# Kernel optimization log

Measured on AMD Instinct MI355X. Metric: run time of the kernel, lower is better.

The kernel has to match this reference:

```python
import math
import jax, jax.numpy as jnp
import numpy as np

D = 512; H = 8; N = 6; DFF = 2048; VS = 32000; VT = 32000
B = 4; S = 1024; T = 1024
EPS = 1e-5


def _pe(length, d):
    pos = jnp.arange(length, dtype=jnp.float32)[:, None]
    div = jnp.exp(jnp.arange(0, d, 2, dtype=jnp.float32) * (-math.log(10000.0) / d))
    pe = jnp.zeros((length, d), jnp.float32)
    pe = pe.at[:, 0::2].set(jnp.sin(pos * div)).at[:, 1::2].set(jnp.cos(pos * div))
    return pe  # [L, D]


def _ln(x, g, b):
    m = x.mean(-1, keepdims=True)
    v = ((x - m) ** 2).mean(-1, keepdims=True)
    return (x - m) / jnp.sqrt(v + EPS) * g + b


def _mha(xq, xkv, w, b, mask):
    # w: [4, D, D], b: [4, D]; mask broadcastable to [B, H, Sq, Sk]
    nb, sq, d = xq.shape
    dk = d // H
    def proj(x, i):
        return (x @ w[i] + b[i]).reshape(x.shape[0], x.shape[1], H, dk).transpose(0, 2, 1, 3)
    q, k, v = proj(xq, 0), proj(xkv, 1), proj(xkv, 2)
    scores = jnp.einsum('bhqd,bhkd->bhqk', q, k) / math.sqrt(dk)
    scores = jnp.where(mask == 0, -1e9, scores)
    p = jax.nn.softmax(scores, axis=-1)
    o = jnp.einsum('bhqk,bhkd->bhqd', p, v).transpose(0, 2, 1, 3).reshape(nb, sq, d)
    return o @ w[3] + b[3]


def _ffn(x, w1, b1, w2, b2):
    return jax.nn.relu(x @ w1 + b1) @ w2 + b2


def _forward(src_emb, tgt_emb,
             enc_attn_w, enc_attn_b, enc_ffn_w1, enc_ffn_b1, enc_ffn_w2, enc_ffn_b2,
             enc_ln_g, enc_ln_b, enc_fg, enc_fb,
             dec_self_w, dec_self_b, dec_src_w, dec_src_b,
             dec_ffn_w1, dec_ffn_b1, dec_ffn_w2, dec_ffn_b2,
             dec_ln_g, dec_ln_b, dec_fg, dec_fb,
             gen_w, gen_b,
             src, tgt, src_mask, tgt_mask):
    # embed + positional encoding (dropout off: eval mode)
    x = src_emb[src] + _pe(src.shape[1], D)[None]
    for i in range(N):
        a = _mha(x, x, enc_attn_w[i], enc_attn_b[i], src_mask)
        x = _ln(x + a, enc_ln_g[i, 0], enc_ln_b[i, 0])
        f = _ffn(x, enc_ffn_w1[i], enc_ffn_b1[i], enc_ffn_w2[i], enc_ffn_b2[i])
        x = _ln(x + f, enc_ln_g[i, 1], enc_ln_b[i, 1])
    memory = _ln(x, enc_fg, enc_fb)

    y = tgt_emb[tgt] + _pe(tgt.shape[1], D)[None]
    for i in range(N):
        a = _mha(y, y, dec_self_w[i], dec_self_b[i], tgt_mask)
        y = _ln(y + a, dec_ln_g[i, 0], dec_ln_b[i, 0])
        a = _mha(y, memory, dec_src_w[i], dec_src_b[i], src_mask)
        y = _ln(y + a, dec_ln_g[i, 1], dec_ln_b[i, 1])
        f = _ffn(y, dec_ffn_w1[i], dec_ffn_b1[i], dec_ffn_w2[i], dec_ffn_b2[i])
        y = _ln(y + f, dec_ln_g[i, 2], dec_ln_b[i, 2])
    y = _ln(y, dec_fg, dec_fb)
    return y @ gen_w + gen_b  # [B, T, VT]


def setup_inputs():
    key = jax.random.key(0)
    ks = iter(jax.random.split(key, 48))
    def w(*shape):
        return jax.random.normal(next(ks), shape, dtype=jnp.float32) * 0.02
    inp = {}
    inp['src_emb'] = w(VS, D)
    inp['tgt_emb'] = w(VT, D)
    inp['enc_attn_w'] = w(N, 4, D, D)
    inp['enc_attn_b'] = jnp.zeros((N, 4, D), jnp.float32)
    inp['enc_ffn_w1'] = w(N, D, DFF)
    inp['enc_ffn_b1'] = jnp.zeros((N, DFF), jnp.float32)
    inp['enc_ffn_w2'] = w(N, DFF, D)
    inp['enc_ffn_b2'] = jnp.zeros((N, D), jnp.float32)
    inp['enc_ln_g'] = jnp.ones((N, 2, D), jnp.float32)
    inp['enc_ln_b'] = jnp.zeros((N, 2, D), jnp.float32)
    inp['enc_fg'] = jnp.ones((D,), jnp.float32)
    inp['enc_fb'] = jnp.zeros((D,), jnp.float32)
    inp['dec_self_w'] = w(N, 4, D, D)
    inp['dec_self_b'] = jnp.zeros((N, 4, D), jnp.float32)
    inp['dec_src_w'] = w(N, 4, D, D)
    inp['dec_src_b'] = jnp.zeros((N, 4, D), jnp.float32)
    inp['dec_ffn_w1'] = w(N, D, DFF)
    inp['dec_ffn_b1'] = jnp.zeros((N, DFF), jnp.float32)
    inp['dec_ffn_w2'] = w(N, DFF, D)
    inp['dec_ffn_b2'] = jnp.zeros((N, D), jnp.float32)
    inp['dec_ln_g'] = jnp.ones((N, 3, D), jnp.float32)
    inp['dec_ln_b'] = jnp.zeros((N, 3, D), jnp.float32)
    inp['dec_fg'] = jnp.ones((D,), jnp.float32)
    inp['dec_fb'] = jnp.zeros((D,), jnp.float32)
    inp['gen_w'] = w(D, VT)
    inp['gen_b'] = jnp.zeros((VT,), jnp.float32)
    inp['src'] = jax.random.randint(next(ks), (B, S), 0, VS)
    inp['tgt'] = jax.random.randint(next(ks), (B, T), 0, VT)
    inp['src_mask'] = jnp.ones((B, 1, 1, S), jnp.int32)
    inp['tgt_mask'] = jnp.tril(jnp.ones((T, T), jnp.int32))[None, None]  # causal [1,1,T,T]
    return inp


def reference(src_emb, tgt_emb, enc_attn_w, enc_attn_b, enc_ffn_w1, enc_ffn_b1,
              enc_ffn_w2, enc_ffn_b2, enc_ln_g, enc_ln_b, enc_fg, enc_fb,
              dec_self_w, dec_self_b, dec_src_w, dec_src_b,
              dec_ffn_w1, dec_ffn_b1, dec_ffn_w2, dec_ffn_b2,
              dec_ln_g, dec_ln_b, dec_fg, dec_fb, gen_w, gen_b,
              src, tgt, src_mask, tgt_mask):
    return _forward(src_emb, tgt_emb, enc_attn_w, enc_attn_b, enc_ffn_w1, enc_ffn_b1,
                    enc_ffn_w2, enc_ffn_b2, enc_ln_g, enc_ln_b, enc_fg, enc_fb,
                    dec_self_w, dec_self_b, dec_src_w, dec_src_b,
                    dec_ffn_w1, dec_ffn_b1, dec_ffn_w2, dec_ffn_b2,
                    dec_ln_g, dec_ln_b, dec_fg, dec_fb, gen_w, gen_b,
                    src, tgt, src_mask, tgt_mask)
```

## Files before the change

### kernel.cpp

```cpp
#include <hip/hip_runtime.h>


typedef __bf16 bf16x8 __attribute__((ext_vector_type(8)));
typedef __bf16 bf16x4 __attribute__((ext_vector_type(4)));
typedef float  f32x4  __attribute__((ext_vector_type(4)));

__device__ __forceinline__ void gload_lds16(const void* g, void* l) {
  __builtin_amdgcn_global_load_lds((__attribute__((address_space(1))) void*)g,
                                   (__attribute__((address_space(3))) void*)l,
                                   16, 0, 0);
}

__device__ __forceinline__ void hard_barrier() {
  asm volatile("" ::: "memory");
  __builtin_amdgcn_sched_barrier(0);
  __builtin_amdgcn_s_barrier();
  __builtin_amdgcn_sched_barrier(0);
  asm volatile("" ::: "memory");
}

__global__ __launch_bounds__(512, 2)
void gemm256_kernel(const __bf16* __restrict__ A, int lda,
                    const __bf16* __restrict__ BT, int ldb,
                    float* __restrict__ C, int ldc,
                    const float* __restrict__ bias, int K)
{
  __shared__ char ldsraw[131072];
  const int tid  = threadIdx.x;
  const int lane = tid & 63, wid = tid >> 6;
  const int wr = wid >> 2, wc = wid & 3;
  const int bm = blockIdx.x * 256, bn = blockIdx.y * 256;

  auto stage = [&](int slot, int kt) {
    const char* Ag = (const char*)A;
    const char* Bg = (const char*)BT;
    char* base = ldsraw + slot * 65536;
    const long long k0b = (long long)kt * 128;
#pragma unroll
    for (int i = 0; i < 4; i++) {
      int t = tid + i * 512;
      int row = t >> 3, cb = (t & 7) << 4;
      int src = cb ^ ((row & 7) << 4);
      gload_lds16(Ag + ((long long)(bm + row) * lda) * 2 + k0b + src, base + t * 16);
    }
#pragma unroll
    for (int i = 0; i < 4; i++) {
      int t = tid + i * 512;
      int row = t >> 3, cb = (t & 7) << 4;
      int src = cb ^ ((row & 7) << 4);
      gload_lds16(Bg + ((long long)(bn + row) * ldb) * 2 + k0b + src,
                  base + 32768 + t * 16);
    }
  };

  f32x4 acc[8][4] = {};
  const int NT = K / 64;

  stage(0, 0);
  stage(1, 1);

  for (int kt = 0; kt < NT; kt++) {
    if (kt < NT - 1) {
      asm volatile("s_waitcnt vmcnt(8)" ::: "memory");
    } else {
      asm volatile("s_waitcnt vmcnt(0)" ::: "memory");
    }
    hard_barrier();
    const char* sA = ldsraw + (kt & 1) * 65536;
    const char* sB = sA + 32768;
#pragma unroll
    for (int q = 0; q < 4; q++) {
      const int qr = q >> 1, qc = q & 1;
      bf16x8 af[4][2], bf[2][2];
#pragma unroll
      for (int i = 0; i < 4; i++) {
        int row = wr * 128 + (qr * 4 + i) * 16 + (lane & 15);
#pragma unroll
        for (int kk = 0; kk < 2; kk++) {
          int g = kk * 64 + (lane >> 4) * 16;
          af[i][kk] = *(const bf16x8*)(sA + row * 128 + (g ^ ((row & 7) << 4)));
        }
      }
#pragma unroll
      for (int j = 0; j < 2; j++) {
        int row = wc * 64 + (qc * 2 + j) * 16 + (lane & 15);
#pragma unroll
        for (int kk = 0; kk < 2; kk++) {
          int g = kk * 64 + (lane >> 4) * 16;
          bf[j][kk] = *(const bf16x8*)(sB + row * 128 + (g ^ ((row & 7) << 4)));
        }
      }
      __builtin_amdgcn_s_barrier();
      asm volatile("s_waitcnt lgkmcnt(0)" ::: "memory");
      __builtin_amdgcn_sched_barrier(0);
      __builtin_amdgcn_s_setprio(1);
#pragma unroll
      for (int kk = 0; kk < 2; kk++)
#pragma unroll
        for (int i = 0; i < 4; i++)
#pragma unroll
          for (int j = 0; j < 2; j++)
            acc[qr * 4 + i][qc * 2 + j] = __builtin_amdgcn_mfma_f32_16x16x32_bf16(
                af[i][kk], bf[j][kk], acc[qr * 4 + i][qc * 2 + j], 0, 0, 0);
      __builtin_amdgcn_s_setprio(0);
    }
    hard_barrier();
    if (kt + 2 < NT) stage(kt & 1, kt + 2);
  }

  float* ct = (float*)ldsraw;
#pragma unroll
  for (int c = 0; c < 4; c++) {
    __syncthreads();
    if (wr == (c >> 1)) {
      const int ib = (c & 1) * 4;
#pragma unroll
      for (int i = 0; i < 4; i++) {
#pragma unroll
        for (int j = 0; j < 4; j++) {
          int lrow = i * 16 + (lane >> 4) * 4;
          int lcol = wc * 64 + j * 16 + (lane & 15);
          float bv = bias[bn + lcol];
#pragma unroll
          for (int r = 0; r < 4; r++)
            ct[(lrow + r) * 260 + lcol] = acc[ib + i][j][r] + bv;
        }
      }
    }
    __syncthreads();
#pragma unroll
    for (int it = 0; it < 8; it++) {
      int idx = tid + it * 512;
      int row = idx >> 6, c4 = (idx & 63) * 4;
      f32x4 v = *(const f32x4*)(ct + row * 260 + c4);
      *(f32x4*)(C + (long long)(bm + c * 64 + row) * ldc + bn + c4) = v;
    }
  }
}

template<int EPI>
__global__ __launch_bounds__(256)
void gemm2_kernel(const __bf16* __restrict__ A, const __bf16* __restrict__ Akv,
                  int lda,
                  const __bf16* __restrict__ BT, int ldb,
                  void* __restrict__ Cv, int ldc,
                  const float* __restrict__ bias, int K,
                  __bf16* __restrict__ qb, __bf16* __restrict__ kb,
                  __bf16* __restrict__ vt)
{
  constexpr int BM = 128, BN = 128, BK = 64;
  constexpr int WM = 64, WN = 64, FM = 4, FN = 4;
  constexpr int SLOT = 2 * BM * BK;
  __shared__ char ldsraw[65536];
  __bf16* lds = (__bf16*)ldsraw;
  const int tid  = threadIdx.x;
  const int lane = tid & 63, wave = tid >> 6;
  const int wr = wave >> 1, wc = wave & 1;
  const int bm = blockIdx.x * BM, bn = blockIdx.y * BN;
  const __bf16* Ause = (EPI == 2 && blockIdx.y >= 4) ? Akv : A;

  auto stage = [&](int slot, int kt) {
    const char* Ag = (const char*)Ause;
    const char* Bg = (const char*)BT;
    char* base = (char*)(lds + slot * SLOT);
    const long long k0b = (long long)kt * (BK * 2);
#pragma unroll
    for (int i = 0; i < 4; i++) {
      int t = tid + i * 256;
      int row = t >> 3, cb = (t & 7) << 4;
      int src = cb ^ ((row & 7) << 4);
      gload_lds16(Ag + ((long long)(bm + row) * lda) * 2 + k0b + src, base + t * 16);
    }
#pragma unroll
    for (int i = 0; i < 4; i++) {
      int t = tid + i * 256;
      int row = t >> 3, cb = (t & 7) << 4;
      int src = cb ^ ((row & 7) << 4);
      gload_lds16(Bg + ((long long)(bn + row) * ldb) * 2 + k0b + src,
                  base + BM * BK * 2 + t * 16);
    }
  };

  f32x4 acc[FM][FN] = {};
  const int NT = K / BK;

  stage(0, 0);
  stage(1, 1);

  for (int t = 0; t < NT; t++) {
    if (t < NT - 1) {
      asm volatile("s_waitcnt vmcnt(8)" ::: "memory");
    } else {
      asm volatile("s_waitcnt vmcnt(0)" ::: "memory");
    }
    hard_barrier();
    const char* sA = (const char*)(lds + (t & 1) * SLOT);
    const char* sB = sA + BM * BK * 2;
#pragma unroll
    for (int kk = 0; kk < 2; kk++) {
      const int g = kk * 64 + (lane >> 4) * 16;
      bf16x8 af[FM], bfr[FN];
#pragma unroll
      for (int i = 0; i < FM; i++) {
        int row = wr * WM + i * 16 + (lane & 15);
        af[i] = *(const bf16x8*)(sA + row * 128 + (g ^ ((row & 7) << 4)));
      }
#pragma unroll
      for (int j = 0; j < FN; j++) {
        int row = wc * WN + j * 16 + (lane & 15);
        bfr[j] = *(const bf16x8*)(sB + row * 128 + (g ^ ((row & 7) << 4)));
      }
      __builtin_amdgcn_s_setprio(1);
#pragma unroll
      for (int i = 0; i < FM; i++)
#pragma unroll
        for (int j = 0; j < FN; j++)
          acc[i][j] = __builtin_amdgcn_mfma_f32_16x16x32_bf16(af[i], bfr[j], acc[i][j], 0, 0, 0);
      __builtin_amdgcn_s_setprio(0);
    }
    hard_barrier();
    if (t + 2 < NT) stage(t & 1, t + 2);
  }

#pragma unroll
  for (int i = 0; i < FM; i++) {
#pragma unroll
    for (int j = 0; j < FN; j++) {
      int row0 = bm + wr * WM + i * 16 + (lane >> 4) * 4;
      int col  = bn + wc * WN + j * 16 + (lane & 15);
      float bv = bias ? bias[col] : 0.f;
      if constexpr (EPI == 2) {
        int z = col >> 9;
        int cw = col & 511;
        int b = row0 >> 10, s = row0 & 1023;
        int h = cw >> 6, dk = cw & 63;
        long long bh = b * 8 + h;
        if (z == 2) {
          bf16x4 vv;
#pragma unroll
          for (int r = 0; r < 4; r++) vv[r] = (__bf16)(acc[i][j][r] + bv);
          *(bf16x4*)(vt + (bh << 16) + (dk << 10) + s) = vv;
        } else {
          __bf16* dst = (z == 0) ? qb : kb;
          float sc = (z == 0) ? 0.125f : 1.0f;
#pragma unroll
          for (int r = 0; r < 4; r++)
            dst[(bh << 16) + ((long long)(s + r) << 6) + dk] = (__bf16)((acc[i][j][r] + bv) * sc);
        }
      } else {
        __bf16* C = (__bf16*)Cv;
#pragma unroll
        for (int r = 0; r < 4; r++)
          C[(long long)(row0 + r) * ldc + col] = (__bf16)fmaxf(acc[i][j][r] + bv, 0.f);
      }
    }
  }
}

__global__ __launch_bounds__(256)
void gemm_kernel(const __bf16* __restrict__ A, int lda,
                 const __bf16* __restrict__ BT, int ldb,
                 const __bf16* __restrict__ Xbase,
                 __bf16* __restrict__ Xs, int ldc,
                 const float* __restrict__ bias, int K)
{
  constexpr int BM = 128, BN = 64, BK = 64;
  constexpr int WM = 64, WN = 32, FM = 4, FN = 2;
  constexpr int LA = (BM * BK) / 2048;
  constexpr int LB = (BN * BK) / 2048;
  constexpr int SLOT = (BM + BN) * BK;
  __shared__ __bf16 lds[3 * SLOT];
  const int tid  = threadIdx.x;
  const int lane = tid & 63, wave = tid >> 6;
  const int wr = wave >> 1, wc = wave & 1;
  const int bm = blockIdx.x * BM, bn = blockIdx.y * BN;

  auto stage = [&](int slot, int kt) {
    const char* Ag = (const char*)A;
    const char* Bg = (const char*)BT;
    char* base = (char*)(lds + slot * SLOT);
    const long long k0b = (long long)kt * (BK * 2);
#pragma unroll
    for (int i = 0; i < LA; i++) {
      int t = tid + i * 256;
      int row = t >> 3, cb = (t & 7) << 4;
      int src = cb ^ ((row & 7) << 4);
      gload_lds16(Ag + ((long long)(bm + row) * lda) * 2 + k0b + src, base + t * 16);
    }
#pragma unroll
    for (int i = 0; i < LB; i++) {
      int t = tid + i * 256;
      int row = t >> 3, cb = (t & 7) << 4;
      int src = cb ^ ((row & 7) << 4);
      gload_lds16(Bg + ((long long)(bn + row) * ldb) * 2 + k0b + src,
                  base + BM * BK * 2 + t * 16);
    }
  };

  f32x4 acc[FM][FN] = {};
  const int NT = K / BK;

  stage(0, 0);
  stage(1, 1);

  for (int t = 0; t < NT; t++) {
    if (t < NT - 1) {
      asm volatile("s_waitcnt vmcnt(6)" ::: "memory");
    } else {
      asm volatile("s_waitcnt vmcnt(0)" ::: "memory");
    }
    hard_barrier();
    if (t + 2 < NT) stage((t + 2) % 3, t + 2);
    const char* sA = (const char*)(lds + (t % 3) * SLOT);
    const char* sB = sA + BM * BK * 2;
#pragma unroll
    for (int kk = 0; kk < 2; kk++) {
      const int g = kk * 64 + (lane >> 4) * 16;
      bf16x8 af[FM], bfr[FN];
#pragma unroll
      for (int i = 0; i < FM; i++) {
        int row = wr * WM + i * 16 + (lane & 15);
        af[i] = *(const bf16x8*)(sA + row * 128 + (g ^ ((row & 7) << 4)));
      }
#pragma unroll
      for (int j = 0; j < FN; j++) {
        int row = wc * WN + j * 16 + (lane & 15);
        bfr[j] = *(const bf16x8*)(sB + row * 128 + (g ^ ((row & 7) << 4)));
      }
      __builtin_amdgcn_s_setprio(1);
#pragma unroll
      for (int i = 0; i < FM; i++)
#pragma unroll
        for (int j = 0; j < FN; j++)
          acc[i][j] = __builtin_amdgcn_mfma_f32_16x16x32_bf16(af[i], bfr[j], acc[i][j], 0, 0, 0);
      __builtin_amdgcn_s_setprio(0);
    }
  }

#pragma unroll
  for (int i = 0; i < FM; i++) {
#pragma unroll
    for (int j = 0; j < FN; j++) {
      int row0 = bm + wr * WM + i * 16 + (lane >> 4) * 4;
      int col  = bn + wc * WN + j * 16 + (lane & 15);
      float bv = bias[col];
#pragma unroll
      for (int r = 0; r < 4; r++) {
        long long off = (long long)(row0 + r) * ldc + col;
        Xs[off] = (__bf16)(acc[i][j][r] + bv + (float)Xbase[off]);
      }
    }
  }
}

template<int CAUSAL>
__global__ __launch_bounds__(256)
void flash_kernel(const __bf16* __restrict__ qb, const __bf16* __restrict__ kb,
                  const __bf16* __restrict__ vt, const int* __restrict__ smask,
                  __bf16* __restrict__ Ob)
{
  __shared__ __bf16 lK[2 * 128 * 64];
  __shared__ __bf16 lV[2 * 64 * 128];
  __shared__ __bf16 lP[4][16 * 128];
  const int bh = blockIdx.y;
  const int b = bh >> 3, h = bh & 7;
  const int qt = CAUSAL ? ((blockIdx.y < 16) ? blockIdx.x : 15 - blockIdx.x)
                        : blockIdx.x;
  const int q0 = qt * 64;
  const int tid = threadIdx.x, lane = tid & 63, w = tid >> 6;
  const char* kh = (const char*)(kb + ((long long)bh << 16));
  const char* vh = (const char*)(vt + ((long long)bh << 16));

  auto stageKV = [&](int buf, int t) {
    int k0 = t * 128;
#pragma unroll
    for (int i = 0; i < 4; i++) {
      int c = tid + i * 256;
      int row = c >> 3, cb = (c & 7) << 4;
      int cl = cb ^ ((row & 7) << 4);
      gload_lds16(kh + (long long)(k0 + row) * 128 + cl, (char*)lK + buf * 16384 + c * 16);
    }
#pragma unroll
    for (int i = 0; i < 4; i++) {
      int c = tid + i * 256;
      int row = c >> 4, cb = (c & 15) << 4;
      int cl = cb ^ ((row & 7) << 4);
      gload_lds16(vh + (long long)row * 2048 + (long long)k0 * 2 + cl, (char*)lV + buf * 16384 + c * 16);
    }
  };

  bf16x8 qa[2];
  {
    const __bf16* qrow = qb + ((long long)bh << 16)
                       + (long long)(q0 + w * 16 + (lane & 15)) * 64 + (lane >> 4) * 8;
    qa[0] = *(const bf16x8*)(qrow);
    qa[1] = *(const bf16x8*)(qrow + 32);
  }
  f32x4 oacc[4] = {};
  float m[4], l[4];
#pragma unroll
  for (int r = 0; r < 4; r++) { m[r] = -3e38f; l[r] = 0.f; }

  const int nt = CAUSAL ? (qt / 2 + 1) : 8;
  char* lPw = (char*)lP + w * 4096;

  stageKV(0, 0);
  if (nt > 1) stageKV(1, 1);

  for (int t = 0; t < nt; t++) {
    const int k0 = t * 128;
    if (t < nt - 1) {
      asm volatile("s_waitcnt vmcnt(8)" ::: "memory");
    } else {
      asm volatile("s_waitcnt vmcnt(0)" ::: "memory");
    }
    hard_barrier();
    char* cK = (char*)lK + (t & 1) * 16384;
    char* cV = (char*)lV + (t & 1) * 16384;

    f32x4 sf[8];
#pragma unroll
    for (int f = 0; f < 8; f++) {
      int row = f * 16 + (lane & 15);
      f32x4 s = {};
#pragma unroll
      for (int ks = 0; ks < 2; ks++) {
        int cb = ks * 64 + (lane >> 4) * 16;
        bf16x8 kf = *(const bf16x8*)(cK + row * 128 + (cb ^ ((row & 7) << 4)));
        s = __builtin_amdgcn_mfma_f32_16x16x32_bf16(qa[ks], kf, s, 0, 0, 0);
      }
      sf[f] = s;
    }

    if (!CAUSAL) {
#pragma unroll
      for (int f = 0; f < 8; f++) {
        if (smask[b * 1024 + k0 + f * 16 + (lane & 15)] == 0) {
#pragma unroll
          for (int r = 0; r < 4; r++) sf[f][r] = -1e30f;
        }
      }
    } else if (t == nt - 1) {
#pragma unroll
      for (int f = 0; f < 8; f++) {
        int kc = k0 + f * 16 + (lane & 15);
#pragma unroll
        for (int r = 0; r < 4; r++) {
          int qr = q0 + w * 16 + (lane >> 4) * 4 + r;
          if (kc > qr) sf[f][r] = -1e30f;
        }
      }
    }

    float mt[4];
#pragma unroll
    for (int r = 0; r < 4; r++) {
      float v = sf[0][r];
#pragma unroll
      for (int f = 1; f < 8; f++) v = fmaxf(v, sf[f][r]);
      mt[r] = v;
    }
#pragma unroll
    for (int o = 1; o < 16; o <<= 1)
#pragma unroll
      for (int r = 0; r < 4; r++) mt[r] = fmaxf(mt[r], __shfl_xor(mt[r], o));

    bool need = false;
#pragma unroll
    for (int r = 0; r < 4; r++) need = need || (mt[r] > m[r] + 8.f);
    if (__any(need)) {
      float mn[4], cr[4];
#pragma unroll
      for (int r = 0; r < 4; r++) {
        mn[r] = fmaxf(m[r], mt[r]);
        cr[r] = __expf(m[r] - mn[r]);
        m[r]  = mn[r];
        l[r] *= cr[r];
      }
#pragma unroll
      for (int d = 0; d < 4; d++)
#pragma unroll
        for (int r = 0; r < 4; r++) oacc[d][r] *= cr[r];
    }
    float rs[4] = {0.f, 0.f, 0.f, 0.f};
#pragma unroll
    for (int f = 0; f < 8; f++)
#pragma unroll
      for (int r = 0; r < 4; r++) {
        float p = __expf(sf[f][r] - m[r]);
        sf[f][r] = p;
        rs[r] += p;
      }
#pragma unroll
    for (int o = 1; o < 16; o <<= 1)
#pragma unroll
      for (int r = 0; r < 4; r++) rs[r] += __shfl_xor(rs[r], o);
#pragma unroll
    for (int r = 0; r < 4; r++) l[r] += rs[r];

#pragma unroll
    for (int f = 0; f < 8; f++) {
      int colB = f * 32 + (lane & 15) * 2;
#pragma unroll
      for (int r = 0; r < 4; r++) {
        int row = (lane >> 4) * 4 + r;
        *(__bf16*)(lPw + row * 256 + (colB ^ ((row & 7) << 4))) = (__bf16)sf[f][r];
      }
    }
    asm volatile("s_waitcnt lgkmcnt(0)" ::: "memory");

#pragma unroll
    for (int ks = 0; ks < 4; ks++) {
      int prow = lane & 15;
      int cb = ks * 64 + (lane >> 4) * 16;
      bf16x8 pa = *(const bf16x8*)(lPw + prow * 256 + (cb ^ ((prow & 7) << 4)));
#pragma unroll
      for (int d = 0; d < 4; d++) {
        int vrow = d * 16 + (lane & 15);
        bf16x8 vf = *(const bf16x8*)(cV + vrow * 256 + (cb ^ ((vrow & 7) << 4)));
        oacc[d] = __builtin_amdgcn_mfma_f32_16x16x32_bf16(pa, vf, oacc[d], 0, 0, 0);
      }
    }
    hard_barrier();
    if (t + 2 < nt) stageKV(t & 1, t + 2);
  }

  float inv[4];
#pragma unroll
  for (int r = 0; r < 4; r++) inv[r] = 1.f / l[r];
#pragma unroll
  for (int d = 0; d < 4; d++)
#pragma unroll
    for (int r = 0; r < 4; r++) {
      long long row = b * 1024 + q0 + w * 16 + (lane >> 4) * 4 + r;
      Ob[row * 512 + h * 64 + d * 16 + (lane & 15)] = (__bf16)(oacc[d][r] * inv[r]);
    }
}

__global__ void transpose_w_kernel(const float* __restrict__ W, __bf16* __restrict__ WT,
                                   int K, int N)
{
  __shared__ float t[32][33];
  long long mz = (long long)blockIdx.z * K * N;
  W += mz; WT += mz;
  int n0 = blockIdx.x * 32, k0 = blockIdx.y * 32;
  int tx = threadIdx.x, ty = threadIdx.y;
#pragma unroll
  for (int i = 0; i < 32; i += 8)
    t[ty + i][tx] = W[(long long)(k0 + ty + i) * N + (n0 + tx)];
  __syncthreads();
#pragma unroll
  for (int i = 0; i < 32; i += 8)
    WT[(long long)(n0 + ty + i) * K + (k0 + tx)] = (__bf16)t[tx][ty + i];
}

__global__ void embed_kernel(const float* __restrict__ emb, const int* __restrict__ idx,
                             __bf16* __restrict__ Xb)
{
  int row = blockIdx.x;
  int s   = row & 1023;
  int tok = idx[row];
  int d0  = threadIdx.x * 4;
  float4 e = *(const float4*)(emb + (long long)tok * 512 + d0);
  const float* ep = (const float*)&e;
  bf16x4 ob;
#pragma unroll
  for (int j = 0; j < 4; j++) {
    int d = d0 + j;
    float div = expf((float)(d & ~1) * (-9.210340371976184f / 512.f));
    float ang = (float)s * div;
    float pe  = (d & 1) ? cosf(ang) : sinf(ang);
    ob[j] = (__bf16)(ep[j] + pe);
  }
  *(bf16x4*)(Xb + (long long)row * 512 + d0) = ob;
}

__global__ __launch_bounds__(256)
void ln_kernel(const __bf16* __restrict__ Xin,
               const float* __restrict__ g, const float* __restrict__ b,
               __bf16* __restrict__ Xbout)
{
  int row = blockIdx.x * 4 + (threadIdx.x >> 6);
  int lane = threadIdx.x & 63;
  long long base = (long long)row * 512 + lane * 8;
  bf16x8 xv = *(const bf16x8*)(Xin + base);
  float x[8];
#pragma unroll
  for (int i = 0; i < 8; i++) x[i] = (float)xv[i];
  float s = 0.f;
#pragma unroll
  for (int i = 0; i < 8; i++) s += x[i];
#pragma unroll
  for (int o = 32; o > 0; o >>= 1) s += __shfl_xor(s, o);
  float mean = s * (1.f / 512.f);
  float v = 0.f;
#pragma unroll
  for (int i = 0; i < 8; i++) { x[i] -= mean; v += x[i] * x[i]; }
#pragma unroll
  for (int o = 32; o > 0; o >>= 1) v += __shfl_xor(v, o);
  float inv = rsqrtf(v * (1.f / 512.f) + 1e-5f);
  int d0 = lane * 8;
  float gg[8], bb[8];
  *(float4*)gg       = *(const float4*)(g + d0);
  *(float4*)(gg + 4) = *(const float4*)(g + d0 + 4);
  *(float4*)bb       = *(const float4*)(b + d0);
  *(float4*)(bb + 4) = *(const float4*)(b + d0 + 4);
  bf16x8 yb;
#pragma unroll
  for (int i = 0; i < 8; i++)
    yb[i] = (__bf16)(x[i] * inv * gg[i] + bb[i]);
  *(bf16x8*)(Xbout + base) = yb;
}

extern "C" void kernel_launch(void* const* d_in, const int* in_sizes, int n_in,
                              void* d_out, int out_size, void* d_ws, size_t ws_size,
                              hipStream_t stream)
{
  (void)in_sizes; (void)n_in; (void)out_size; (void)ws_size;
  const float* src_emb    = (const float*)d_in[0];
  const float* tgt_emb    = (const float*)d_in[1];
  const float* enc_attn_w = (const float*)d_in[2];
  const float* enc_attn_b = (const float*)d_in[3];
  const float* enc_ffn_w1 = (const float*)d_in[4];
  const float* enc_ffn_b1 = (const float*)d_in[5];
  const float* enc_ffn_w2 = (const float*)d_in[6];
  const float* enc_ffn_b2 = (const float*)d_in[7];
  const float* enc_ln_g   = (const float*)d_in[8];
  const float* enc_ln_b   = (const float*)d_in[9];
  const float* enc_fg     = (const float*)d_in[10];
  const float* enc_fb     = (const float*)d_in[11];
  const float* dec_self_w = (const float*)d_in[12];
  const float* dec_self_b = (const float*)d_in[13];
  const float* dec_src_w  = (const float*)d_in[14];
  const float* dec_src_b  = (const float*)d_in[15];
  const float* dec_ffn_w1 = (const float*)d_in[16];
  const float* dec_ffn_b1 = (const float*)d_in[17];
  const float* dec_ffn_w2 = (const float*)d_in[18];
  const float* dec_ffn_b2 = (const float*)d_in[19];
  const float* dec_ln_g   = (const float*)d_in[20];
  const float* dec_ln_b   = (const float*)d_in[21];
  const float* dec_fg     = (const float*)d_in[22];
  const float* dec_fb     = (const float*)d_in[23];
  const float* gen_w      = (const float*)d_in[24];
  const float* gen_b      = (const float*)d_in[25];
  const int*   src        = (const int*)d_in[26];
  const int*   tgt        = (const int*)d_in[27];
  const int*   src_mask   = (const int*)d_in[28];

  float* out = (float*)d_out;

  char* wp = (char*)d_ws;
  auto alloc = [&](size_t bytes) { void* p = (void*)wp; wp += (bytes + 255) & ~(size_t)255; return p; };
  __bf16* TWea = (__bf16*)alloc(24ull * 262144 * 2);
  __bf16* TWe1 = (__bf16*)alloc(6ull * 1048576 * 2);
  __bf16* TWe2 = (__bf16*)alloc(6ull * 1048576 * 2);
  __bf16* TWds = (__bf16*)alloc(24ull * 262144 * 2);
  __bf16* TWdx = (__bf16*)alloc(24ull * 262144 * 2);
  __bf16* TWd1 = (__bf16*)alloc(6ull * 1048576 * 2);
  __bf16* TWd2 = (__bf16*)alloc(6ull * 1048576 * 2);
  __bf16* Xb   = (__bf16*)alloc(4096ull * 512 * 2);
  __bf16* MEMb = (__bf16*)alloc(4096ull * 512 * 2);
  __bf16* Xs   = (__bf16*)alloc(4096ull * 512 * 2);
  __bf16* qb   = (__bf16*)alloc(32ull * 1024 * 64 * 2);
  __bf16* kb   = (__bf16*)alloc(32ull * 1024 * 64 * 2);
  __bf16* vt   = (__bf16*)alloc(32ull * 1024 * 64 * 2);
  __bf16* Ob   = (__bf16*)alloc(4096ull * 512 * 2);
  __bf16* Fb   = qb;
  __bf16* GENT = TWea;

  transpose_w_kernel<<<dim3(16, 16, 24), dim3(32, 8), 0, stream>>>(enc_attn_w, TWea, 512, 512);
  transpose_w_kernel<<<dim3(64, 16, 6),  dim3(32, 8), 0, stream>>>(enc_ffn_w1, TWe1, 512, 2048);
  transpose_w_kernel<<<dim3(16, 64, 6),  dim3(32, 8), 0, stream>>>(enc_ffn_w2, TWe2, 2048, 512);
  transpose_w_kernel<<<dim3(16, 16, 24), dim3(32, 8), 0, stream>>>(dec_self_w, TWds, 512, 512);
  transpose_w_kernel<<<dim3(16, 16, 24), dim3(32, 8), 0, stream>>>(dec_src_w,  TWdx, 512, 512);
  transpose_w_kernel<<<dim3(64, 16, 6),  dim3(32, 8), 0, stream>>>(dec_ffn_w1, TWd1, 512, 2048);
  transpose_w_kernel<<<dim3(16, 64, 6),  dim3(32, 8), 0, stream>>>(dec_ffn_w2, TWd2, 2048, 512);

  auto attention = [&](const __bf16* wt, const float* bptr, int causal,
                       const __bf16* Aq, const __bf16* Akv) {
    gemm2_kernel<2><<<dim3(32, 12), 256, 0, stream>>>(
        Aq, Akv, 512, wt, 512, nullptr, 0, bptr, 512, qb, kb, vt);
    if (causal)
      flash_kernel<1><<<dim3(16, 32), 256, 0, stream>>>(qb, kb, vt, nullptr, Ob);
    else
      flash_kernel<0><<<dim3(16, 32), 256, 0, stream>>>(qb, kb, vt, src_mask, Ob);
    gemm_kernel<<<dim3(32, 8), 256, 0, stream>>>(
        Ob, 512, wt + 3 * 262144, 512, Xb, Xs, 512, bptr + 3 * 512, 512);
  };

  auto ffn = [&](const __bf16* w1t, const float* b1, const __bf16* w2t, const float* b2) {
    gemm2_kernel<1><<<dim3(32, 16), 256, 0, stream>>>(
        Xb, Xb, 512, w1t, 512, Fb, 2048, b1, 512, nullptr, nullptr, nullptr);
    gemm_kernel<<<dim3(32, 8), 256, 0, stream>>>(
        Fb, 2048, w2t, 2048, Xb, Xs, 512, b2, 2048);
  };

  embed_kernel<<<4096, 128, 0, stream>>>(src_emb, src, Xb);
  for (int i = 0; i < 6; i++) {
    attention(TWea + (long long)i * 1048576, enc_attn_b + i * 2048, 0, Xb, Xb);
    ln_kernel<<<1024, 256, 0, stream>>>(Xs, enc_ln_g + i * 1024, enc_ln_b + i * 1024, Xb);
    ffn(TWe1 + (long long)i * 1048576, enc_ffn_b1 + i * 2048,
        TWe2 + (long long)i * 1048576, enc_ffn_b2 + i * 512);
    ln_kernel<<<1024, 256, 0, stream>>>(Xs, enc_ln_g + i * 1024 + 512, enc_ln_b + i * 1024 + 512, Xb);
  }
  ln_kernel<<<1024, 256, 0, stream>>>(Xb, enc_fg, enc_fb, MEMb);

  transpose_w_kernel<<<dim3(1000, 16, 1), dim3(32, 8), 0, stream>>>(gen_w, GENT, 512, 32000);

  embed_kernel<<<4096, 128, 0, stream>>>(tgt_emb, tgt, Xb);
  for (int i = 0; i < 6; i++) {
    attention(TWds + (long long)i * 1048576, dec_self_b + i * 2048, 1, Xb, Xb);
    ln_kernel<<<1024, 256, 0, stream>>>(Xs, dec_ln_g + i * 1536, dec_ln_b + i * 1536, Xb);

    attention(TWdx + (long long)i * 1048576, dec_src_b + i * 2048, 0, Xb, MEMb);
    ln_kernel<<<1024, 256, 0, stream>>>(Xs, dec_ln_g + i * 1536 + 512, dec_ln_b + i * 1536 + 512, Xb);

    ffn(TWd1 + (long long)i * 1048576, dec_ffn_b1 + i * 2048,
        TWd2 + (long long)i * 1048576, dec_ffn_b2 + i * 512);
    ln_kernel<<<1024, 256, 0, stream>>>(Xs, dec_ln_g + i * 1536 + 1024, dec_ln_b + i * 1536 + 1024, Xb);
  }
  ln_kernel<<<1024, 256, 0, stream>>>(Xb, dec_fg, dec_fb, Xb);

  gemm256_kernel<<<dim3(16, 125), 512, 0, stream>>>(
      Xb, 512, GENT, 512, out, 32000, gen_b, 512);
}
```

Measured before the change: 1.783 ms.

## Replace pipelined GEMMs with smaller-tile single-buffered kernels

Swaps the 256x256 double-buffered generator GEMM for a 128x128 single-buffered kernel, and replaces the 128x64 triple-buffered residual GEMM with a 64x64 single-buffered kernel launched on twice as many blocks. The intent is more blocks and higher occupancy for the small N=512 projections and the vocabulary projection. The trade-off is losing software pipelining (load/compute overlap), barrier-based priority scheduling, and data reuse per tile, so each K step now stalls on global loads.

```diff
diff --git a/kernel.cpp b/kernel.cpp
--- a/kernel.cpp
+++ b/kernel.cpp
@@ -19,101 +19,75 @@
   asm volatile("" ::: "memory");
 }
 
-__global__ __launch_bounds__(512, 2)
-void gemm256_kernel(const __bf16* __restrict__ A, int lda,
-                    const __bf16* __restrict__ BT, int ldb,
-                    float* __restrict__ C, int ldc,
-                    const float* __restrict__ bias, int K)
-{
-  __shared__ char ldsraw[131072];
+__global__ __launch_bounds__(256)
+void gemm_gen_kernel(const __bf16* __restrict__ A, int lda,
+                     const __bf16* __restrict__ BT, int ldb,
+                     float* __restrict__ C, int ldc,
+                     const float* __restrict__ bias, int K)
+{
+  __shared__ char ldsraw[34816];
   const int tid  = threadIdx.x;
-  const int lane = tid & 63, wid = tid >> 6;
-  const int wr = wid >> 2, wc = wid & 3;
-  const int bm = blockIdx.x * 256, bn = blockIdx.y * 256;
-
-  auto stage = [&](int slot, int kt) {
+  const int lane = tid & 63, wave = tid >> 6;
+  const int wr = wave >> 1, wc = wave & 1;
+  const int bm = blockIdx.x * 128, bn = blockIdx.y * 128;
+
+  auto stage = [&](int kt) {
     const char* Ag = (const char*)A;
     const char* Bg = (const char*)BT;
-    char* base = ldsraw + slot * 65536;
     const long long k0b = (long long)kt * 128;
 #pragma unroll
     for (int i = 0; i < 4; i++) {
-      int t = tid + i * 512;
+      int t = tid + i * 256;
       int row = t >> 3, cb = (t & 7) << 4;
       int src = cb ^ ((row & 7) << 4);
-      gload_lds16(Ag + ((long long)(bm + row) * lda) * 2 + k0b + src, base + t * 16);
+      gload_lds16(Ag + ((long long)(bm + row) * lda) * 2 + k0b + src, ldsraw + t * 16);
     }
 #pragma unroll
     for (int i = 0; i < 4; i++) {
-      int t = tid + i * 512;
+      int t = tid + i * 256;
       int row = t >> 3, cb = (t & 7) << 4;
       int src = cb ^ ((row & 7) << 4);
       gload_lds16(Bg + ((long long)(bn + row) * ldb) * 2 + k0b + src,
-                  base + 32768 + t * 16);
+                  ldsraw + 16384 + t * 16);
     }
   };
 
-  f32x4 acc[8][4] = {};
+  f32x4 acc[4][4] = {};
   const int NT = K / 64;
 
-  stage(0, 0);
-  stage(1, 1);
-
-  for (int kt = 0; kt < NT; kt++) {
-    if (kt < NT - 1) {
-      asm volatile("s_waitcnt vmcnt(8)" ::: "memory");
-    } else {
-      asm volatile("s_waitcnt vmcnt(0)" ::: "memory");
-    }
-    hard_barrier();
-    const char* sA = ldsraw + (kt & 1) * 65536;
-    const char* sB = sA + 32768;
-#pragma unroll
-    for (int q = 0; q < 4; q++) {
-      const int qr = q >> 1, qc = q & 1;
-      bf16x8 af[4][2], bf[2][2];
+  for (int t = 0; t < NT; t++) {
+    __syncthreads();
+    stage(t);
+    __syncthreads();
+    const char* sA = ldsraw;
+    const char* sB = ldsraw + 16384;
+#pragma unroll
+    for (int kk = 0; kk < 2; kk++) {
+      const int g = kk * 64 + (lane >> 4) * 16;
+      bf16x8 af[4], bfr[4];
 #pragma unroll
       for (int i = 0; i < 4; i++) {
-        int row = wr * 128 + (qr * 4 + i) * 16 + (lane & 15);
-#pragma unroll
-        for (int kk = 0; kk < 2; kk++) {
-          int g = kk * 64 + (lane >> 4) * 16;
-          af[i][kk] = *(const bf16x8*)(sA + row * 128 + (g ^ ((row & 7) << 4)));
-        }
-      }
-#pragma unroll
-      for (int j = 0; j < 2; j++) {
-        int row = wc * 64 + (qc * 2 + j) * 16 + (lane & 15);
-#pragma unroll
-        for (int kk = 0; kk < 2; kk++) {
-          int g = kk * 64 + (lane >> 4) * 16;
-          bf[j][kk] = *(const bf16x8*)(sB + row * 128 + (g ^ ((row & 7) << 4)));
-        }
-      }
-      __builtin_amdgcn_s_barrier();
-      asm volatile("s_waitcnt lgkmcnt(0)" ::: "memory");
-      __builtin_amdgcn_sched_barrier(0);
-      __builtin_amdgcn_s_setprio(1);
-#pragma unroll
-      for (int kk = 0; kk < 2; kk++)
-#pragma unroll
-        for (int i = 0; i < 4; i++)
-#pragma unroll
-          for (int j = 0; j < 2; j++)
-            acc[qr * 4 + i][qc * 2 + j] = __builtin_amdgcn_mfma_f32_16x16x32_bf16(
-                af[i][kk], bf[j][kk], acc[qr * 4 + i][qc * 2 + j], 0, 0, 0);
-      __builtin_amdgcn_s_setprio(0);
-    }
-    hard_barrier();
-    if (kt + 2 < NT) stage(kt & 1, kt + 2);
+        int row = wr * 64 + i * 16 + (lane & 15);
+        af[i] = *(const bf16x8*)(sA + row * 128 + (g ^ ((row & 7) << 4)));
+      }
+#pragma unroll
+      for (int j = 0; j < 4; j++) {
+        int row = wc * 64 + j * 16 + (lane & 15);
+        bfr[j] = *(const bf16x8*)(sB + row * 128 + (g ^ ((row & 7) << 4)));
+      }
+#pragma unroll
+      for (int i = 0; i < 4; i++)
+#pragma unroll
+        for (int j = 0; j < 4; j++)
+          acc[i][j] = __builtin_amdgcn_mfma_f32_16x16x32_bf16(af[i], bfr[j], acc[i][j], 0, 0, 0);
+    }
   }
 
   float* ct = (float*)ldsraw;
 #pragma unroll
-  for (int c = 0; c < 4; c++) {
+  for (int c = 0; c < 2; c++) {
     __syncthreads();
-    if (wr == (c >> 1)) {
-      const int ib = (c & 1) * 4;
+    if (wr == c) {
 #pragma unroll
       for (int i = 0; i < 4; i++) {
 #pragma unroll
@@ -123,17 +97,98 @@
           float bv = bias[bn + lcol];
 #pragma unroll
           for (int r = 0; r < 4; r++)
-            ct[(lrow + r) * 260 + lcol] = acc[ib + i][j][r] + bv;
+            ct[(lrow + r) * 132 + lcol] = acc[i][j][r] + bv;
         }
       }
     }
     __syncthreads();
 #pragma unroll
     for (int it = 0; it < 8; it++) {
-      int idx = tid + it * 512;
-      int row = idx >> 6, c4 = (idx & 63) * 4;
-      f32x4 v = *(const f32x4*)(ct + row * 260 + c4);
+      int idx = tid + it * 256;
+      int row = idx >> 5, c4 = (idx & 31) * 4;
+      f32x4 v = *(const f32x4*)(ct + row * 132 + c4);
       *(f32x4*)(C + (long long)(bm + c * 64 + row) * ldc + bn + c4) = v;
+    }
+  }
+}
+
+__global__ __launch_bounds__(256)
+void gemm64_kernel(const __bf16* __restrict__ A, int lda,
+                   const __bf16* __restrict__ BT, int ldb,
+                   const __bf16* __restrict__ Xbase,
+                   __bf16* __restrict__ Xs, int ldc,
+                   const float* __restrict__ bias, int K)
+{
+  __shared__ char ldsraw[16384];
+  const int tid  = threadIdx.x;
+  const int lane = tid & 63, wave = tid >> 6;
+  const int wr = wave >> 1, wc = wave & 1;
+  const int bm = blockIdx.x * 64, bn = blockIdx.y * 64;
+
+  auto stage = [&](int kt) {
+    const char* Ag = (const char*)A;
+    const char* Bg = (const char*)BT;
+    const long long k0b = (long long)kt * 128;
+#pragma unroll
+    for (int i = 0; i < 2; i++) {
+      int t = tid + i * 256;
+      int row = t >> 3, cb = (t & 7) << 4;
+      int src = cb ^ ((row & 7) << 4);
+      gload_lds16(Ag + ((long long)(bm + row) * lda) * 2 + k0b + src, ldsraw + t * 16);
+    }
+#pragma unroll
+    for (int i = 0; i < 2; i++) {
+      int t = tid + i * 256;
+      int row = t >> 3, cb = (t & 7) << 4;
+      int src = cb ^ ((row & 7) << 4);
+      gload_lds16(Bg + ((long long)(bn + row) * ldb) * 2 + k0b + src,
+                  ldsraw + 8192 + t * 16);
+    }
+  };
+
+  f32x4 acc[2][2] = {};
+  const int NT = K / 64;
+
+  for (int t = 0; t < NT; t++) {
+    __syncthreads();
+    stage(t);
+    __syncthreads();
+    const char* sA = ldsraw;
+    const char* sB = ldsraw + 8192;
+#pragma unroll
+    for (int kk = 0; kk < 2; kk++) {
+      const int g = kk * 64 + (lane >> 4) * 16;
+      bf16x8 af[2], bfr[2];
+#pragma unroll
+      for (int i = 0; i < 2; i++) {
+        int row = wr * 32 + i * 16 + (lane & 15);
+        af[i] = *(const bf16x8*)(sA + row * 128 + (g ^ ((row & 7) << 4)));
+      }
+#pragma unroll
+      for (int j = 0; j < 2; j++) {
+        int row = wc * 32 + j * 16 + (lane & 15);
+        bfr[j] = *(const bf16x8*)(sB + row * 128 + (g ^ ((row & 7) << 4)));
+      }
+#pragma unroll
+      for (int i = 0; i < 2; i++)
+#pragma unroll
+        for (int j = 0; j < 2; j++)
+          acc[i][j] = __builtin_amdgcn_mfma_f32_16x16x32_bf16(af[i], bfr[j], acc[i][j], 0, 0, 0);
+    }
+  }
+
+#pragma unroll
+  for (int i = 0; i < 2; i++) {
+#pragma unroll
+    for (int j = 0; j < 2; j++) {
+      int row0 = bm + wr * 32 + i * 16 + (lane >> 4) * 4;
+      int col  = bn + wc * 32 + j * 16 + (lane & 15);
+      float bv = bias[col];
+#pragma unroll
+      for (int r = 0; r < 4; r++) {
+        long long off = (long long)(row0 + r) * ldc + col;
+        Xs[off] = (__bf16)(acc[i][j][r] + bv + (float)Xbase[off]);
+      }
     }
   }
 }
@@ -252,102 +307,6 @@
 #pragma unroll
         for (int r = 0; r < 4; r++)
           C[(long long)(row0 + r) * ldc + col] = (__bf16)fmaxf(acc[i][j][r] + bv, 0.f);
-      }
-    }
-  }
-}
-
-__global__ __launch_bounds__(256)
-void gemm_kernel(const __bf16* __restrict__ A, int lda,
-                 const __bf16* __restrict__ BT, int ldb,
-                 const __bf16* __restrict__ Xbase,
-                 __bf16* __restrict__ Xs, int ldc,
-                 const float* __restrict__ bias, int K)
-{
-  constexpr int BM = 128, BN = 64, BK = 64;
-  constexpr int WM = 64, WN = 32, FM = 4, FN = 2;
-  constexpr int LA = (BM * BK) / 2048;
-  constexpr int LB = (BN * BK) / 2048;
-  constexpr int SLOT = (BM + BN) * BK;
-  __shared__ __bf16 lds[3 * SLOT];
-  const int tid  = threadIdx.x;
-  const int lane = tid & 63, wave = tid >> 6;
-  const int wr = wave >> 1, wc = wave & 1;
-  const int bm = blockIdx.x * BM, bn = blockIdx.y * BN;
-
-  auto stage = [&](int slot, int kt) {
-    const char* Ag = (const char*)A;
-    const char* Bg = (const char*)BT;
-    char* base = (char*)(lds + slot * SLOT);
-    const long long k0b = (long long)kt * (BK * 2);
-#pragma unroll
-    for (int i = 0; i < LA; i++) {
-      int t = tid + i * 256;
-      int row = t >> 3, cb = (t & 7) << 4;
-      int src = cb ^ ((row & 7) << 4);
-      gload_lds16(Ag + ((long long)(bm + row) * lda) * 2 + k0b + src, base + t * 16);
-    }
-#pragma unroll
-    for (int i = 0; i < LB; i++) {
-      int t = tid + i * 256;
-      int row = t >> 3, cb = (t & 7) << 4;
-      int src = cb ^ ((row & 7) << 4);
-      gload_lds16(Bg + ((long long)(bn + row) * ldb) * 2 + k0b + src,
-                  base + BM * BK * 2 + t * 16);
-    }
-  };
-
-  f32x4 acc[FM][FN] = {};
-  const int NT = K / BK;
-
-  stage(0, 0);
-  stage(1, 1);
-
-  for (int t = 0; t < NT; t++) {
-    if (t < NT - 1) {
-      asm volatile("s_waitcnt vmcnt(6)" ::: "memory");
-    } else {
-      asm volatile("s_waitcnt vmcnt(0)" ::: "memory");
-    }
-    hard_barrier();
-    if (t + 2 < NT) stage((t + 2) % 3, t + 2);
-    const char* sA = (const char*)(lds + (t % 3) * SLOT);
-    const char* sB = sA + BM * BK * 2;
-#pragma unroll
-    for (int kk = 0; kk < 2; kk++) {
-      const int g = kk * 64 + (lane >> 4) * 16;
-      bf16x8 af[FM], bfr[FN];
-#pragma unroll
-      for (int i = 0; i < FM; i++) {
-        int row = wr * WM + i * 16 + (lane & 15);
-        af[i] = *(const bf16x8*)(sA + row * 128 + (g ^ ((row & 7) << 4)));
-      }
-#pragma unroll
-      for (int j = 0; j < FN; j++) {
-        int row = wc * WN + j * 16 + (lane & 15);
-        bfr[j] = *(const bf16x8*)(sB + row * 128 + (g ^ ((row & 7) << 4)));
-      }
-      __builtin_amdgcn_s_setprio(1);
-#pragma unroll
-      for (int i = 0; i < FM; i++)
-#pragma unroll
-        for (int j = 0; j < FN; j++)
-          acc[i][j] = __builtin_amdgcn_mfma_f32_16x16x32_bf16(af[i], bfr[j], acc[i][j], 0, 0, 0);
-      __builtin_amdgcn_s_setprio(0);
-    }
-  }
-
-#pragma unroll
-  for (int i = 0; i < FM; i++) {
-#pragma unroll
-    for (int j = 0; j < FN; j++) {
-      int row0 = bm + wr * WM + i * 16 + (lane >> 4) * 4;
-      int col  = bn + wc * WN + j * 16 + (lane & 15);
-      float bv = bias[col];
-#pragma unroll
-      for (int r = 0; r < 4; r++) {
-        long long off = (long long)(row0 + r) * ldc + col;
-        Xs[off] = (__bf16)(acc[i][j][r] + bv + (float)Xbase[off]);
       }
     }
   }
@@ -684,14 +643,14 @@
       flash_kernel<1><<<dim3(16, 32), 256, 0, stream>>>(qb, kb, vt, nullptr, Ob);
     else
       flash_kernel<0><<<dim3(16, 32), 256, 0, stream>>>(qb, kb, vt, src_mask, Ob);
-    gemm_kernel<<<dim3(32, 8), 256, 0, stream>>>(
+    gemm64_kernel<<<dim3(64, 8), 256, 0, stream>>>(
         Ob, 512, wt + 3 * 262144, 512, Xb, Xs, 512, bptr + 3 * 512, 512);
   };
 
   auto ffn = [&](const __bf16* w1t, const float* b1, const __bf16* w2t, const float* b2) {
     gemm2_kernel<1><<<dim3(32, 16), 256, 0, stream>>>(
         Xb, Xb, 512, w1t, 512, Fb, 2048, b1, 512, nullptr, nullptr, nullptr);
-    gemm_kernel<<<dim3(32, 8), 256, 0, stream>>>(
+    gemm64_kernel<<<dim3(64, 8), 256, 0, stream>>>(
         Fb, 2048, w2t, 2048, Xb, Xs, 512, b2, 2048);
   };
 
@@ -721,6 +680,6 @@
   }
   ln_kernel<<<1024, 256, 0, stream>>>(Xb, dec_fg, dec_fb, Xb);
 
-  gemm256_kernel<<<dim3(16, 125), 512, 0, stream>>>(
+  gemm_gen_kernel<<<dim3(32, 250), 256, 0, stream>>>(
       Xb, 512, GENT, 512, out, 32000, gen_b, 512);
 }
```

Result: slower. 1.926 ms (+8.0%).
